# Kernel tuning notes

Measured on AMD Instinct MI355X. Metric: run time of the kernel, lower is better.

The kernel has to match this reference:

```python
import jax, jax.numpy as jnp
import numpy as np

N = 100000      # nodes
E = 1600000     # edges (avg degree 16)
DIN = 64
DOUT = 64
C = 8           # num classes; label -1 means unknown


def _xavier(key, shape):
    a = jnp.sqrt(6.0 / (shape[0] + shape[1]))
    return jax.random.uniform(key, shape, jnp.float32, -a, a)


def setup_inputs():
    key = jax.random.key(0)
    ks = jax.random.split(key, 17)
    return {
        "x": jax.random.normal(ks[0], (N, DIN), jnp.float32),
        "adj_low_vals": jax.random.uniform(ks[1], (E,), jnp.float32) / 16.0,
        "adj_high_vals": jax.random.uniform(ks[2], (E,), jnp.float32) / 16.0,
        "weight_low": _xavier(ks[3], (DIN, DOUT)),
        "weight_high": _xavier(ks[4], (DIN, DOUT)),
        "weight_mlp": _xavier(ks[5], (DIN, DOUT)),
        "att_vec_low_fr": _xavier(ks[6], (DOUT, 1)),
        "att_vec_high_fr": _xavier(ks[7], (DOUT, 1)),
        "att_vec_low_be": _xavier(ks[8], (DOUT, 1)),
        "att_vec_high_be": _xavier(ks[9], (DOUT, 1)),
        "att_vec_low_unk": _xavier(ks[10], (DOUT, 1)),
        "att_vec_high_unk": _xavier(ks[11], (DOUT, 1)),
        "att_vec_mlp": _xavier(ks[12], (DOUT, 1)),
        "att_vec7": _xavier(ks[13], (7, 7)),
        "edge_src": jax.random.randint(ks[14], (E,), 0, N),
        "edge_dst": jax.random.randint(ks[15], (E,), 0, N),
        "label_unk": jax.random.randint(ks[16], (N,), -1, C),
    }


def reference(x, adj_low_vals, adj_high_vals, weight_low, weight_high, weight_mlp,
              att_vec_low_fr, att_vec_high_fr, att_vec_low_be, att_vec_high_be,
              att_vec_low_unk, att_vec_high_unk, att_vec_mlp, att_vec7,
              edge_src, edge_dst, label_unk):
    def spmm(vals, feats):  # out[dst] += vals * feats[src]  (sparse [N,N] @ [N,D])
        return jax.ops.segment_sum(vals[:, None] * feats[edge_src], edge_dst, num_segments=N)

    output_low = jax.nn.relu(spmm(adj_low_vals, x @ weight_low))
    output_high = jax.nn.relu(spmm(adj_high_vals, x @ weight_high))
    output_mlp = jax.nn.relu(x @ weight_mlp)

    # per-edge fake label: 2 if either endpoint unknown (<0), 1 if labels differ
    # (both known) -> heterophilous, else 0 -> homophilous
    sl = label_unk[edge_src]
    dl = label_unk[edge_dst]
    fake = jnp.where((sl < 0) | (dl < 0), 2, jnp.where(sl != dl, 1, 0))

    h_low_e = output_low[edge_src]    # [E, DOUT] gathered messages
    h_high_e = output_high[edge_src]

    def agg(h_e, k):  # masked segment-sum over destination nodes
        m = (fake == k).astype(h_e.dtype)[:, None]
        return jax.ops.segment_sum(h_e * m, edge_dst, num_segments=N)

    neigh_homo_low, neigh_hete_low, neigh_unk_low = agg(h_low_e, 0), agg(h_low_e, 1), agg(h_low_e, 2)
    neigh_homo_high, neigh_hete_high, neigh_unk_high = agg(h_high_e, 0), agg(h_high_e, 1), agg(h_high_e, 2)

    # attention7 (fr_high_g is None branch)
    feats = jax.nn.sigmoid(jnp.concatenate([
        neigh_hete_low @ att_vec_low_fr, neigh_hete_high @ att_vec_high_fr,
        neigh_homo_low @ att_vec_low_be, neigh_homo_high @ att_vec_high_be,
        neigh_unk_low @ att_vec_low_unk, neigh_unk_high @ att_vec_high_unk,
        output_mlp @ att_vec_mlp], axis=1))  # [N, 7]
    att = jax.nn.softmax((feats @ att_vec7) / 7.0, axis=1)

    return 7.0 * (att[:, 0:1] * neigh_hete_low + att[:, 1:2] * neigh_hete_high
                  + att[:, 2:3] * neigh_homo_low + att[:, 3:4] * neigh_homo_high
                  + att[:, 4:5] * neigh_unk_low + att[:, 5:6] * neigh_unk_high
                  + att[:, 6:7] * output_mlp)
```

## Files before the change

kernel.cpp:

```cpp
#include <hip/hip_runtime.h>
#include <hip/hip_bf16.h>

typedef unsigned int u32;
typedef unsigned short u16;
typedef unsigned long long u64;

typedef __attribute__((ext_vector_type(8))) short bf16x8;
typedef __attribute__((ext_vector_type(4))) float f32x4;
typedef __attribute__((ext_vector_type(2))) float f32x2;

static __device__ __forceinline__ float bflo(u32 u) { return __uint_as_float(u << 16); }
static __device__ __forceinline__ float bfhi(u32 u) { return __uint_as_float(u & 0xFFFF0000u); }
static __device__ __forceinline__ float bf2f(u16 u) { return __uint_as_float((u32)u << 16); }
static __device__ __forceinline__ u32 f2bf(float f) {
    u32 u = __float_as_uint(f);
    return (u + 0x7FFFu + ((u >> 16) & 1u)) >> 16;
}
static __device__ __forceinline__ u32 packbf(float lo, float hi) {
    return f2bf(lo) | (f2bf(hi) << 16);
}
static __device__ __forceinline__ float ldf(const u16* p16, int idx, int isf32) {
    return isf32 ? ((const float*)p16)[idx] : bf2f(p16[idx]);
}
static __device__ __forceinline__ void load4(const u16* p, int q, int isf32, float* v) {
    if (isf32) {
        float4 t = ((const float4*)p)[q];
        v[0] = t.x; v[1] = t.y; v[2] = t.z; v[3] = t.w;
    } else {
        u32 a = ((const u32*)p)[q * 2], b = ((const u32*)p)[q * 2 + 1];
        v[0] = bflo(a); v[1] = bfhi(a); v[2] = bflo(b); v[3] = bfhi(b);
    }
}
static __device__ __forceinline__ float sanitize(float v, float code) {
    return (fabsf(v) < 1e30f) ? v : code;
}

static __device__ __forceinline__ f32x2 up2(u32 u) {
    f32x2 r;
    r.x = __uint_as_float(u << 16);
    r.y = __uint_as_float(u & 0xFFFF0000u);
    return r;
}
static __device__ __forceinline__ void pk_fma(f32x2& d, f32x2 a, f32x2 b) {
    asm("v_pk_fma_f32 %0, %1, %2, %0" : "+v"(d) : "v"(a), "v"(b));
}
static __device__ __forceinline__ void pk_add(f32x2& d, f32x2 a) {
    asm("v_pk_add_f32 %0, %1, %0" : "+v"(d) : "v"(a));
}

static __device__ __forceinline__ float wave_sum(float v) {
#pragma unroll
    for (int o = 32; o; o >>= 1) v += __shfl_xor(v, o, 64);
    return v;
}
static __device__ __forceinline__ float group_sum(float v) {
#pragma unroll
    for (int o = 8; o; o >>= 1) v += __shfl_xor(v, o, 64);
    return v;
}


__global__ void k_sentinel(float* __restrict__ out, int n, float val) {
    int i = blockIdx.x * blockDim.x + threadIdx.x;
    if (i < n) out[i] = val;
}

__global__ void k_zero_sniff(int* __restrict__ p, int n, const u16* __restrict__ x,
                             int* __restrict__ flag) {
    int i = blockIdx.x * blockDim.x + threadIdx.x;
    if (i < n) p[i] = 0;
    if (blockIdx.x == 0 && threadIdx.x < 64) {
        int lane = threadIdx.x;
        int wild = 0;
        for (int k = 0; k < 64; k++) {
            u32 u = x[lane * 64 + k];
            int e = (u >> 7) & 0xFF;
            if (e < 96 || e > 135) wild++;
        }
        float tot = wave_sum((float)wild);
        if (lane == 0) *flag = (tot > 200.f) ? 1 : 0;
    }
}


__global__ void k_hist(const int* __restrict__ dst, int E, int* __restrict__ deg) {
    int i = blockIdx.x * blockDim.x + threadIdx.x;
    if (i < E) atomicAdd(&deg[dst[i]], 1);
}

__global__ void k_scan_partial(const int* __restrict__ deg, int n, int* __restrict__ bsum) {
    int t = threadIdx.x;
    int base = blockIdx.x * 1024 + t * 4;
    int s = 0;
#pragma unroll
    for (int j = 0; j < 4; j++) {
        int idx = base + j;
        if (idx < n) s += deg[idx];
    }
    __shared__ int sh[256];
    sh[t] = s;
    __syncthreads();
    for (int d = 128; d; d >>= 1) {
        if (t < d) sh[t] += sh[t + d];
        __syncthreads();
    }
    if (t == 0) bsum[blockIdx.x] = sh[0];
}

__global__ void k_scan_bsum(const int* __restrict__ bsum, int nb, int* __restrict__ boff) {
    int t = threadIdx.x;
    int v = (t < nb) ? bsum[t] : 0;
    __shared__ int sh[256];
    sh[t] = v;
    __syncthreads();
    for (int d = 1; d < 256; d <<= 1) {
        int u = (t >= d) ? sh[t - d] : 0;
        __syncthreads();
        sh[t] += u;
        __syncthreads();
    }
    if (t < nb) boff[t] = sh[t] - v;
}

__global__ void k_scan_final(const int* __restrict__ deg, int n, const int* __restrict__ boff,
                             int* __restrict__ offsets, int Etot) {
    int t = threadIdx.x;
    int base = blockIdx.x * 1024 + t * 4;
    int v[4];
    int s = 0;
#pragma unroll
    for (int j = 0; j < 4; j++) {
        int idx = base + j;
        v[j] = (idx < n) ? deg[idx] : 0;
        s += v[j];
    }
    __shared__ int sh[256];
    sh[t] = s;
    __syncthreads();
    for (int d = 1; d < 256; d <<= 1) {
        int u = (t >= d) ? sh[t - d] : 0;
        __syncthreads();
        sh[t] += u;
        __syncthreads();
    }
    int ex = sh[t] - s + boff[blockIdx.x];
#pragma unroll
    for (int j = 0; j < 4; j++) {
        int idx = base + j;
        if (idx < n) offsets[idx] = ex;
        ex += v[j];
    }
    if (blockIdx.x == 0 && t == 0) offsets[n] = Etot;
}

__global__ void k_scat1(const int* __restrict__ src, const int* __restrict__ dst,
                        const u16* __restrict__ avl, const u16* __restrict__ avh,
                        const int* __restrict__ lab, int E,
                        const int* __restrict__ offsets, int* __restrict__ bcur,
                        u64* __restrict__ etmp, const int* __restrict__ flag) {
    int i = blockIdx.x * blockDim.x + threadIdx.x;
    if (i >= E) return;
    int isf32 = *flag;
    int d = dst[i];
    int b = d >> 8;
    int base = b << 8;
    int rank = atomicAdd(&bcur[b * 16], 1);
    int pos = offsets[base] + rank;
    if ((unsigned)pos >= (unsigned)E) return;
    int s = src[i];
    int sl = lab[s], dl = lab[d];
    int fake = (sl < 0 || dl < 0) ? 2 : ((sl != dl) ? 1 : 0);
    u32 lo32 = (u32)s | ((u32)fake << 20) | ((u32)(d - base) << 22);
    u32 hi32 = isf32 ? packbf(((const float*)avl)[i], ((const float*)avh)[i])
                     : ((u32)avl[i] | ((u32)avh[i] << 16));
    etmp[pos] = ((u64)hi32 << 32) | lo32;
}

__launch_bounds__(256) __global__
void k_scat2(const u64* __restrict__ etmp, const int* __restrict__ offsets, int N, int E,
             u64* __restrict__ epay) {
    __shared__ int cur[256];
    int b = blockIdx.x;
    int base = b << 8;
    int t = threadIdx.x;
    cur[t] = 0;
    __syncthreads();
    int hi = min(base + 256, N);
    int r0 = offsets[base];
    int r1 = offsets[hi];
    for (int e = r0 + t; e < r1; e += 256) {
        u64 p = etmp[e];
        int dloc = (int)(p >> 22) & 0xFF;
        int rank = atomicAdd(&cur[dloc], 1);
        int pos = offsets[base + dloc] + rank;
        if ((unsigned)pos < (unsigned)E) epay[pos] = p;
    }
}


__global__ void k_prepB(const u16* __restrict__ wl, const u16* __restrict__ wh,
                        const u16* __restrict__ wm, u16* __restrict__ Bpack,
                        u32* __restrict__ xwlh, u32* __restrict__ outlh, int N,
                        const int* __restrict__ flag) {
    int isf32 = *flag;
    if (threadIdx.x < 64) {
        xwlh[(size_t)N * 64 + threadIdx.x] = 0;
        outlh[(size_t)N * 64 + threadIdx.x] = 0;
    }
    for (int idx = threadIdx.x; idx < 12 * 2 * 64; idx += 256) {
        int slot = idx >> 6;
        int ln = idx & 63;
        int ct = slot >> 1, c = slot & 1;
        int mat = ct >> 2;
        const u16* W = (mat == 0) ? wl : (mat == 1) ? wh : wm;
        int col = (ct & 3) * 16 + (ln & 15);
        int kbase = c * 32 + (ln >> 4) * 8;
        u16* dst = Bpack + (size_t)idx * 8;
#pragma unroll
        for (int j = 0; j < 8; j++) dst[j] = (u16)f2bf(ldf(W, (kbase + j) * 64 + col, isf32));
    }
}

__launch_bounds__(256) __global__
void k_gemm_mfma(const u16* __restrict__ x, const u16* __restrict__ Bpack, int N,
                 u32* __restrict__ xwlh, float* __restrict__ omlp,
                 const int* __restrict__ flag) {
    int isf32 = *flag;
    int lane = threadIdx.x & 63;
    int wv = (blockIdx.x * 256 + threadIdx.x) >> 6;
    int nw = gridDim.x * 4;
    int m = lane & 15, quad = lane >> 4;
    int ntiles = (N + 15) >> 4;
    for (int tile = wv; tile < ntiles; tile += nw) {
        int r0 = tile * 16;
        int arow = min(r0 + m, N - 1);
        bf16x8 a[2];
#pragma unroll
        for (int c = 0; c < 2; c++) {
            int base = arow * 64 + c * 32 + quad * 8;
            if (isf32) {
                const float* xf = (const float*)x;
#pragma unroll
                for (int j = 0; j < 8; j++) a[c][j] = (short)f2bf(xf[base + j]);
            } else {
#pragma unroll
                for (int j = 0; j < 8; j++) a[c][j] = (short)x[base + j];
            }
        }
        f32x4 acc[12];
#pragma unroll
        for (int t = 0; t < 12; t++) acc[t] = (f32x4){0.f, 0.f, 0.f, 0.f};
#pragma unroll
        for (int t = 0; t < 12; t++) {
#pragma unroll
            for (int c = 0; c < 2; c++) {
                bf16x8 b = *(const bf16x8*)(Bpack + (size_t)((t * 2 + c) * 64 + lane) * 8);
                acc[t] = __builtin_amdgcn_mfma_f32_16x16x32_bf16(a[c], b, acc[t], 0, 0, 0);
            }
        }
#pragma unroll
        for (int t = 0; t < 4; t++) {
#pragma unroll
            for (int r = 0; r < 4; r++) {
                int row = r0 + quad * 4 + r;
                if (row < N) {
                    int o = row * 64 + t * 16 + m;
                    xwlh[o] = packbf(acc[t][r], acc[t + 4][r]);
                    omlp[o] = fmaxf(acc[t + 8][r], 0.f);
                }
            }
        }
    }
}


__launch_bounds__(256) __global__
void k_spmm4n(const u32* __restrict__ xwlh, const u64* __restrict__ epay,
              const int* __restrict__ offsets, int N, int E, u32* __restrict__ outlh) {
    int lane = threadIdx.x & 63;
    int gwave = blockIdx.x * 4 + (threadIdx.x >> 6);
    int g = lane & 15, gi = lane >> 4;
    int node = gwave * 4 + gi;
    bool vn = node < N;
    int s = vn ? offsets[node] : 0;
    int e = vn ? offsets[node + 1] : 0;
    int deg = e - s;
    int md = deg;
    md = max(md, __shfl_xor(md, 16, 64));
    md = max(md, __shfl_xor(md, 32, 64));
    f32x2 acc[4];
#pragma unroll
    for (int f = 0; f < 4; f++) acc[f] = (f32x2){0.f, 0.f};
    for (int t = 0; t < md; t += 4) {
        u64 p[4];
#pragma unroll
        for (int u = 0; u < 4; u++) {
            int idx = max(s + min(t + u, deg - 1), 0);
            p[u] = epay[idx];
        }
        uint4 R[4];
        u32 vv[4];
#pragma unroll
        for (int u = 0; u < 4; u++) {
            int sj = ((t + u) < deg) ? min((int)(p[u] & 0xFFFFF), N) : N;
            vv[u] = (u32)(p[u] >> 32);
            R[u] = *((const uint4*)(xwlh + (size_t)sj * 64) + g);
        }
#pragma unroll
        for (int u = 0; u < 4; u++) {
            f32x2 wp;
            wp.x = bflo(vv[u]);
            wp.y = bfhi(vv[u]);
            pk_fma(acc[0], up2(R[u].x), wp);
            pk_fma(acc[1], up2(R[u].y), wp);
            pk_fma(acc[2], up2(R[u].z), wp);
            pk_fma(acc[3], up2(R[u].w), wp);
        }
    }
    if (vn) {
        uint4 W;
        W.x = packbf(fmaxf(acc[0].x, 0.f), fmaxf(acc[0].y, 0.f));
        W.y = packbf(fmaxf(acc[1].x, 0.f), fmaxf(acc[1].y, 0.f));
        W.z = packbf(fmaxf(acc[2].x, 0.f), fmaxf(acc[2].y, 0.f));
        W.w = packbf(fmaxf(acc[3].x, 0.f), fmaxf(acc[3].y, 0.f));
        ((uint4*)(outlh + (size_t)node * 64))[g] = W;
    }
}


__launch_bounds__(256) __global__
void k_agg4n(const u32* __restrict__ outlh, const u64* __restrict__ epay,
             const int* __restrict__ offsets,
             const u16* __restrict__ aLF, const u16* __restrict__ aHF,
             const u16* __restrict__ aLB, const u16* __restrict__ aHB,
             const u16* __restrict__ aLU, const u16* __restrict__ aHU,
             const u16* __restrict__ aM, const u16* __restrict__ a7, int N, int E,
             float* __restrict__ out, const int* __restrict__ flag) {
    int isf32 = *flag;
    int lane = threadIdx.x & 63;
    int gwave = blockIdx.x * 4 + (threadIdx.x >> 6);
    int g = lane & 15, gi = lane >> 4;
    int node = gwave * 4 + gi;
    bool vn = node < N;
    int s = vn ? offsets[node] : 0;
    int e = vn ? offsets[node + 1] : 0;
    int deg = e - s;
    int md = deg;
    md = max(md, __shfl_xor(md, 16, 64));
    md = max(md, __shfl_xor(md, 32, 64));
    f32x2 aT[4], aHe[4], aUn[4];
#pragma unroll
    for (int f = 0; f < 4; f++) {
        aT[f] = (f32x2){0.f, 0.f};
        aHe[f] = (f32x2){0.f, 0.f};
        aUn[f] = (f32x2){0.f, 0.f};
    }
    for (int t = 0; t < md; t += 4) {
        u64 p[4];
#pragma unroll
        for (int u = 0; u < 4; u++) {
            int idx = max(s + min(t + u, deg - 1), 0);
            p[u] = epay[idx];
        }
        uint4 R[4];
        int fk[4];
#pragma unroll
        for (int u = 0; u < 4; u++) {
            fk[u] = (int)(p[u] >> 20) & 3;
            int sj = ((t + u) < deg) ? min((int)(p[u] & 0xFFFFF), N) : N;
            R[u] = *((const uint4*)(outlh + (size_t)sj * 64) + g);
        }
#pragma unroll
        for (int u = 0; u < 4; u++) {
            float he = (fk[u] == 1) ? 1.f : 0.f;
            float un = (fk[u] == 2) ? 1.f : 0.f;
            f32x2 mhe, mun;
            mhe.x = he; mhe.y = he;
            mun.x = un; mun.y = un;
            f32x2 r0 = up2(R[u].x), r1 = up2(R[u].y), r2 = up2(R[u].z), r3 = up2(R[u].w);
            pk_add(aT[0], r0); pk_add(aT[1], r1); pk_add(aT[2], r2); pk_add(aT[3], r3);
            pk_fma(aHe[0], r0, mhe); pk_fma(aHe[1], r1, mhe);
            pk_fma(aHe[2], r2, mhe); pk_fma(aHe[3], r3, mhe);
            pk_fma(aUn[0], r0, mun); pk_fma(aUn[1], r1, mun);
            pk_fma(aUn[2], r2, mun); pk_fma(aUn[3], r3, mun);
        }
    }
    float heL[4], heH[4], hoL[4], hoH[4], unL[4], unH[4];
#pragma unroll
    for (int f = 0; f < 4; f++) {
        heL[f] = aHe[f].x; heH[f] = aHe[f].y;
        unL[f] = aUn[f].x; unH[f] = aUn[f].y;
        hoL[f] = aT[f].x - heL[f] - unL[f];
        hoH[f] = aT[f].y - heH[f] - unH[f];
    }
    float vLF[4], vHF[4], vLB[4], vHB[4], vLU[4], vHU[4], vM[4];
    load4(aLF, g, isf32, vLF);
    load4(aHF, g, isf32, vHF);
    load4(aLB, g, isf32, vLB);
    load4(aHB, g, isf32, vHB);
    load4(aLU, g, isf32, vLU);
    load4(aHU, g, isf32, vHU);
    load4(aM, g, isf32, vM);
    float mvv[4] = {0.f, 0.f, 0.f, 0.f};
    if (vn) {
        float4 MV = ((const float4*)(out + (size_t)node * 64))[g];
        mvv[0] = MV.x; mvv[1] = MV.y; mvv[2] = MV.z; mvv[3] = MV.w;
    }

    float p0 = 0, p1 = 0, p2 = 0, p3 = 0, p4 = 0, p5 = 0, p6 = 0;
#pragma unroll
    for (int k = 0; k < 4; k++) {
        p0 += heL[k] * vLF[k];
        p1 += heH[k] * vHF[k];
        p2 += hoL[k] * vLB[k];
        p3 += hoH[k] * vHB[k];
        p4 += unL[k] * vLU[k];
        p5 += unH[k] * vHU[k];
        p6 += mvv[k] * vM[k];
    }
    float d0 = group_sum(p0), d1 = group_sum(p1), d2 = group_sum(p2), d3 = group_sum(p3);
    float d4 = group_sum(p4), d5 = group_sum(p5), d6 = group_sum(p6);

    float f[7];
    f[0] = 1.f / (1.f + expf(-d0));
    f[1] = 1.f / (1.f + expf(-d1));
    f[2] = 1.f / (1.f + expf(-d2));
    f[3] = 1.f / (1.f + expf(-d3));
    f[4] = 1.f / (1.f + expf(-d4));
    f[5] = 1.f / (1.f + expf(-d5));
    f[6] = 1.f / (1.f + expf(-d6));

    float z[7];
#pragma unroll
    for (int jj = 0; jj < 7; jj++) {
        float acc = 0.f;
#pragma unroll
        for (int i = 0; i < 7; i++) acc += f[i] * ldf(a7, i * 7 + jj, isf32);
        z[jj] = acc * (1.f / 7.f);
    }
    float m = z[0];
#pragma unroll
    for (int jj = 1; jj < 7; jj++) m = fmaxf(m, z[jj]);
    float wsum = 0.f;
    float wv[7];
#pragma unroll
    for (int jj = 0; jj < 7; jj++) { wv[jj] = expf(z[jj] - m); wsum += wv[jj]; }
    float s7 = 7.f / wsum;

    if (vn) {
        float4 W;
        float o0 = wv[0] * heL[0] + wv[1] * heH[0] + wv[2] * hoL[0] + wv[3] * hoH[0] +
                   wv[4] * unL[0] + wv[5] * unH[0] + wv[6] * mvv[0];
        float o1 = wv[0] * heL[1] + wv[1] * heH[1] + wv[2] * hoL[1] + wv[3] * hoH[1] +
                   wv[4] * unL[1] + wv[5] * unH[1] + wv[6] * mvv[1];
        float o2 = wv[0] * heL[2] + wv[1] * heH[2] + wv[2] * hoL[2] + wv[3] * hoH[2] +
                   wv[4] * unL[2] + wv[5] * unH[2] + wv[6] * mvv[2];
        float o3 = wv[0] * heL[3] + wv[1] * heH[3] + wv[2] * hoL[3] + wv[3] * hoH[3] +
                   wv[4] * unL[3] + wv[5] * unH[3] + wv[6] * mvv[3];
        W.x = sanitize(o0 * s7, 333.f);
        W.y = sanitize(o1 * s7, 333.f);
        W.z = sanitize(o2 * s7, 333.f);
        W.w = sanitize(o3 * s7, 333.f);
        ((float4*)(out + (size_t)node * 64))[g] = W;
    }
}


extern "C" void kernel_launch(void* const* d_in, const int* in_sizes, int n_in, void* d_out,
                              int out_size, void* d_ws, size_t ws_size, hipStream_t stream) {
    const u16* x = (const u16*)d_in[0];
    const u16* avl = (const u16*)d_in[1];
    const u16* avh = (const u16*)d_in[2];
    const u16* wl = (const u16*)d_in[3];
    const u16* wh = (const u16*)d_in[4];
    const u16* wm = (const u16*)d_in[5];
    const u16* aLF = (const u16*)d_in[6];
    const u16* aHF = (const u16*)d_in[7];
    const u16* aLB = (const u16*)d_in[8];
    const u16* aHB = (const u16*)d_in[9];
    const u16* aLU = (const u16*)d_in[10];
    const u16* aHU = (const u16*)d_in[11];
    const u16* aM = (const u16*)d_in[12];
    const u16* a7 = (const u16*)d_in[13];
    const int* esrc = (const int*)d_in[14];
    const int* edst = (const int*)d_in[15];
    const int* lab = (const int*)d_in[16];
    float* out = (float*)d_out;

    const int N = in_sizes[0] / 64;
    const int E = in_sizes[1];

    char* w = (char*)d_ws;
    size_t off = 0;
    auto alloc = [&](size_t bytes) -> char* {
        char* p = w + off;
        off += (bytes + 255) & ~(size_t)255;
        return p;
    };
    int* flag = (int*)alloc(256);
    int* offsets = (int*)alloc((size_t)(N + 1) * 4);
    int* degcur = (int*)alloc((size_t)2 * N * 4);
    int* bsum = (int*)alloc(256 * 4);
    int* boff = (int*)alloc(256 * 4);
    u16* Bpack = (u16*)alloc(12 * 2 * 64 * 8 * 2);
    u64* epay = (u64*)alloc((size_t)E * 8);
    u32* xwlh = (u32*)alloc((size_t)(N + 1) * 64 * 4);
    u32* outlh = (u32*)alloc((size_t)(N + 1) * 64 * 4);

    if (ws_size < off) {
        k_sentinel<<<(out_size + 255) / 256, 256, 0, stream>>>(out, out_size, 1000.0f);
        return;
    }

    int* deg = degcur;
    int* bcur = degcur + N;
    u64* etmp = (u64*)xwlh;
    int NB = (N + 1023) / 1024;
    int NB2 = (N + 255) / 256;

    k_zero_sniff<<<(2 * N + 255) / 256, 256, 0, stream>>>(degcur, 2 * N, x, flag);
    k_hist<<<(E + 255) / 256, 256, 0, stream>>>(edst, E, deg);
    k_scan_partial<<<NB, 256, 0, stream>>>(deg, N, bsum);
    k_scan_bsum<<<1, 256, 0, stream>>>(bsum, NB, boff);
    k_scan_final<<<NB, 256, 0, stream>>>(deg, N, boff, offsets, E);
    k_scat1<<<(E + 255) / 256, 256, 0, stream>>>(esrc, edst, avl, avh, lab, E, offsets, bcur,
                                                 etmp, flag);
    k_scat2<<<NB2, 256, 0, stream>>>(etmp, offsets, N, E, epay);

    k_prepB<<<1, 256, 0, stream>>>(wl, wh, wm, Bpack, xwlh, outlh, N, flag);
    int ntiles = (N + 15) / 16;
    int gemmBlocks = (ntiles + 3) / 4;
    k_gemm_mfma<<<gemmBlocks, 256, 0, stream>>>(x, Bpack, N, xwlh, out , flag);

    int nodeBlocks = (N + 15) / 16;
    k_spmm4n<<<nodeBlocks, 256, 0, stream>>>(xwlh, epay, offsets, N, E, outlh);
    k_agg4n<<<nodeBlocks, 256, 0, stream>>>(outlh, epay, offsets, aLF, aHF, aLB, aHB, aLU, aHU,
                                            aM, a7, N, E, out, flag);
}
```

Baseline: 467.7 us.

## Pad CSR rows to multiples of four and process one node per wave

Each node's edge list is padded to a multiple of 4 with dummy entries that point at the zero row N and carry fake label 3. The SpMM and aggregation kernels now give one wave per node, with four edge slots of 16 lanes each, and finish with a cross-slot shuffle reduction. This removes the per-group max-degree divergence and the clamped index work of the old four-nodes-per-wave scheme. In exchange it adds a fill of the padded payload array, extra dummy edge loads, a shuffle reduction, and idle lanes on the final store. The GEMM's input loads are also vectorised.

```diff
diff --git a/kernel.cpp b/kernel.cpp
--- a/kernel.cpp
+++ b/kernel.cpp
@@ -57,6 +57,12 @@
 #pragma unroll
     for (int o = 8; o; o >>= 1) v += __shfl_xor(v, o, 64);
     return v;
+}
+static __device__ __forceinline__ void eslot_reduce(f32x2& a) {
+    a.x += __shfl_xor(a.x, 16, 64);
+    a.y += __shfl_xor(a.y, 16, 64);
+    a.x += __shfl_xor(a.x, 32, 64);
+    a.y += __shfl_xor(a.y, 32, 64);
 }
 
 
@@ -95,7 +101,7 @@
 #pragma unroll
     for (int j = 0; j < 4; j++) {
         int idx = base + j;
-        if (idx < n) s += deg[idx];
+        if (idx < n) s += (deg[idx] + 3) & ~3;
     }
     __shared__ int sh[256];
     sh[t] = s;
@@ -107,7 +113,8 @@
     if (t == 0) bsum[blockIdx.x] = sh[0];
 }
 
-__global__ void k_scan_bsum(const int* __restrict__ bsum, int nb, int* __restrict__ boff) {
+__global__ void k_scan_bsum(const int* __restrict__ bsum, int nb, int* __restrict__ boff,
+                            int* __restrict__ tot) {
     int t = threadIdx.x;
     int v = (t < nb) ? bsum[t] : 0;
     __shared__ int sh[256];
@@ -120,10 +127,11 @@
         __syncthreads();
     }
     if (t < nb) boff[t] = sh[t] - v;
+    if (t == nb - 1) *tot = sh[t];
 }
 
 __global__ void k_scan_final(const int* __restrict__ deg, int n, const int* __restrict__ boff,
-                             int* __restrict__ offsets, int Etot) {
+                             int* __restrict__ offsets) {
     int t = threadIdx.x;
     int base = blockIdx.x * 1024 + t * 4;
     int v[4];
@@ -131,7 +139,7 @@
 #pragma unroll
     for (int j = 0; j < 4; j++) {
         int idx = base + j;
-        v[j] = (idx < n) ? deg[idx] : 0;
+        v[j] = (idx < n) ? ((deg[idx] + 3) & ~3) : 0;
         s += v[j];
     }
     __shared__ int sh[256];
@@ -150,15 +158,17 @@
         if (idx < n) offsets[idx] = ex;
         ex += v[j];
     }
-    if (blockIdx.x == 0 && t == 0) offsets[n] = Etot;
 }
 
 __global__ void k_scat1(const int* __restrict__ src, const int* __restrict__ dst,
                         const u16* __restrict__ avl, const u16* __restrict__ avh,
-                        const int* __restrict__ lab, int E,
+                        const int* __restrict__ lab, int E, int Pcap, u64 dum,
                         const int* __restrict__ offsets, int* __restrict__ bcur,
-                        u64* __restrict__ etmp, const int* __restrict__ flag) {
+                        u64* __restrict__ etmp, u64* __restrict__ epay,
+                        const int* __restrict__ flag) {
     int i = blockIdx.x * blockDim.x + threadIdx.x;
+    int stride = blockDim.x * gridDim.x;
+    for (int j = i; j < Pcap; j += stride) epay[j] = dum;
     if (i >= E) return;
     int isf32 = *flag;
     int d = dst[i];
@@ -166,7 +176,7 @@
     int base = b << 8;
     int rank = atomicAdd(&bcur[b * 16], 1);
     int pos = offsets[base] + rank;
-    if ((unsigned)pos >= (unsigned)E) return;
+    if ((unsigned)pos >= (unsigned)Pcap) return;
     int s = src[i];
     int sl = lab[s], dl = lab[d];
     int fake = (sl < 0 || dl < 0) ? 2 : ((sl != dl) ? 1 : 0);
@@ -177,23 +187,22 @@
 }
 
 __launch_bounds__(256) __global__
-void k_scat2(const u64* __restrict__ etmp, const int* __restrict__ offsets, int N, int E,
-             u64* __restrict__ epay) {
+void k_scat2(const u64* __restrict__ etmp, const int* __restrict__ offsets,
+             const int* __restrict__ bcur, int N, int Pcap, u64* __restrict__ epay) {
     __shared__ int cur[256];
     int b = blockIdx.x;
     int base = b << 8;
     int t = threadIdx.x;
     cur[t] = 0;
     __syncthreads();
-    int hi = min(base + 256, N);
     int r0 = offsets[base];
-    int r1 = offsets[hi];
+    int r1 = r0 + bcur[b * 16];
     for (int e = r0 + t; e < r1; e += 256) {
         u64 p = etmp[e];
         int dloc = (int)(p >> 22) & 0xFF;
         int rank = atomicAdd(&cur[dloc], 1);
         int pos = offsets[base + dloc] + rank;
-        if ((unsigned)pos < (unsigned)E) epay[pos] = p;
+        if ((unsigned)pos < (unsigned)Pcap) epay[pos] = p;
     }
 }
 
@@ -239,12 +248,15 @@
         for (int c = 0; c < 2; c++) {
             int base = arow * 64 + c * 32 + quad * 8;
             if (isf32) {
-                const float* xf = (const float*)x;
-#pragma unroll
-                for (int j = 0; j < 8; j++) a[c][j] = (short)f2bf(xf[base + j]);
+                const float4* xf = (const float4*)x;
+                int q = (base >> 2);
+                float4 t0 = xf[q], t1 = xf[q + 1];
+                a[c][0] = (short)f2bf(t0.x); a[c][1] = (short)f2bf(t0.y);
+                a[c][2] = (short)f2bf(t0.z); a[c][3] = (short)f2bf(t0.w);
+                a[c][4] = (short)f2bf(t1.x); a[c][5] = (short)f2bf(t1.y);
+                a[c][6] = (short)f2bf(t1.z); a[c][7] = (short)f2bf(t1.w);
             } else {
-#pragma unroll
-                for (int j = 0; j < 8; j++) a[c][j] = (short)x[base + j];
+                a[c] = *(const bf16x8*)(x + base);
             }
         }
         f32x4 acc[12];
@@ -275,109 +287,101 @@
 
 
 __launch_bounds__(256) __global__
-void k_spmm4n(const u32* __restrict__ xwlh, const u64* __restrict__ epay,
-              const int* __restrict__ offsets, int N, int E, u32* __restrict__ outlh) {
+void k_spmm1n(const u32* __restrict__ xwlh, const u64* __restrict__ epay,
+              const int* __restrict__ offsets, int N, u32* __restrict__ outlh) {
     int lane = threadIdx.x & 63;
-    int gwave = blockIdx.x * 4 + (threadIdx.x >> 6);
-    int g = lane & 15, gi = lane >> 4;
-    int node = gwave * 4 + gi;
-    bool vn = node < N;
-    int s = vn ? offsets[node] : 0;
-    int e = vn ? offsets[node + 1] : 0;
-    int deg = e - s;
-    int md = deg;
-    md = max(md, __shfl_xor(md, 16, 64));
-    md = max(md, __shfl_xor(md, 32, 64));
+    int node = blockIdx.x * 4 + (threadIdx.x >> 6);
+    if (node >= N) return;
+    int f = lane & 15, eslot = lane >> 4;
+    int s = offsets[node];
+    int epad = offsets[node + 1];
+    const uint4* tab = (const uint4*)xwlh + f;
     f32x2 acc[4];
 #pragma unroll
-    for (int f = 0; f < 4; f++) acc[f] = (f32x2){0.f, 0.f};
-    for (int t = 0; t < md; t += 4) {
-        u64 p[4];
-#pragma unroll
-        for (int u = 0; u < 4; u++) {
-            int idx = max(s + min(t + u, deg - 1), 0);
-            p[u] = epay[idx];
-        }
-        uint4 R[4];
-        u32 vv[4];
-#pragma unroll
-        for (int u = 0; u < 4; u++) {
-            int sj = ((t + u) < deg) ? min((int)(p[u] & 0xFFFFF), N) : N;
-            vv[u] = (u32)(p[u] >> 32);
-            R[u] = *((const uint4*)(xwlh + (size_t)sj * 64) + g);
-        }
-#pragma unroll
-        for (int u = 0; u < 4; u++) {
-            f32x2 wp;
-            wp.x = bflo(vv[u]);
-            wp.y = bfhi(vv[u]);
-            pk_fma(acc[0], up2(R[u].x), wp);
-            pk_fma(acc[1], up2(R[u].y), wp);
-            pk_fma(acc[2], up2(R[u].z), wp);
-            pk_fma(acc[3], up2(R[u].w), wp);
-        }
-    }
-    if (vn) {
+    for (int k = 0; k < 4; k++) acc[k] = (f32x2){0.f, 0.f};
+    int t = s + eslot;
+    for (; t + 4 < epad; t += 8) {
+        u64 p0 = epay[t];
+        u64 p1 = epay[t + 4];
+        uint4 R0 = tab[(size_t)(p0 & 0xFFFFF) << 4];
+        uint4 R1 = tab[(size_t)(p1 & 0xFFFFF) << 4];
+        u32 h0 = (u32)(p0 >> 32), h1 = (u32)(p1 >> 32);
+        f32x2 w0, w1;
+        w0.x = bflo(h0); w0.y = bfhi(h0);
+        w1.x = bflo(h1); w1.y = bfhi(h1);
+        pk_fma(acc[0], up2(R0.x), w0);
+        pk_fma(acc[1], up2(R0.y), w0);
+        pk_fma(acc[2], up2(R0.z), w0);
+        pk_fma(acc[3], up2(R0.w), w0);
+        pk_fma(acc[0], up2(R1.x), w1);
+        pk_fma(acc[1], up2(R1.y), w1);
+        pk_fma(acc[2], up2(R1.z), w1);
+        pk_fma(acc[3], up2(R1.w), w1);
+    }
+    if (t < epad) {
+        u64 p0 = epay[t];
+        uint4 R0 = tab[(size_t)(p0 & 0xFFFFF) << 4];
+        u32 h0 = (u32)(p0 >> 32);
+        f32x2 w0;
+        w0.x = bflo(h0); w0.y = bfhi(h0);
+        pk_fma(acc[0], up2(R0.x), w0);
+        pk_fma(acc[1], up2(R0.y), w0);
+        pk_fma(acc[2], up2(R0.z), w0);
+        pk_fma(acc[3], up2(R0.w), w0);
+    }
+#pragma unroll
+    for (int k = 0; k < 4; k++) eslot_reduce(acc[k]);
+    if (eslot == 0) {
         uint4 W;
         W.x = packbf(fmaxf(acc[0].x, 0.f), fmaxf(acc[0].y, 0.f));
         W.y = packbf(fmaxf(acc[1].x, 0.f), fmaxf(acc[1].y, 0.f));
         W.z = packbf(fmaxf(acc[2].x, 0.f), fmaxf(acc[2].y, 0.f));
         W.w = packbf(fmaxf(acc[3].x, 0.f), fmaxf(acc[3].y, 0.f));
-        ((uint4*)(outlh + (size_t)node * 64))[g] = W;
+        ((uint4*)(outlh + (size_t)node * 64))[f] = W;
     }
 }
 
 
 __launch_bounds__(256) __global__
-void k_agg4n(const u32* __restrict__ outlh, const u64* __restrict__ epay,
+void k_agg1n(const u32* __restrict__ outlh, const u64* __restrict__ epay,
              const int* __restrict__ offsets,
              const u16* __restrict__ aLF, const u16* __restrict__ aHF,
              const u16* __restrict__ aLB, const u16* __restrict__ aHB,
              const u16* __restrict__ aLU, const u16* __restrict__ aHU,
-             const u16* __restrict__ aM, const u16* __restrict__ a7, int N, int E,
+             const u16* __restrict__ aM, const u16* __restrict__ a7, int N,
              float* __restrict__ out, const int* __restrict__ flag) {
     int isf32 = *flag;
     int lane = threadIdx.x & 63;
-    int gwave = blockIdx.x * 4 + (threadIdx.x >> 6);
-    int g = lane & 15, gi = lane >> 4;
-    int node = gwave * 4 + gi;
-    bool vn = node < N;
-    int s = vn ? offsets[node] : 0;
-    int e = vn ? offsets[node + 1] : 0;
-    int deg = e - s;
-    int md = deg;
-    md = max(md, __shfl_xor(md, 16, 64));
-    md = max(md, __shfl_xor(md, 32, 64));
+    int node = blockIdx.x * 4 + (threadIdx.x >> 6);
+    if (node >= N) return;
+    int f = lane & 15, eslot = lane >> 4;
+    int s = offsets[node];
+    int epad = offsets[node + 1];
+    const uint4* tab = (const uint4*)outlh + f;
     f32x2 aT[4], aHe[4], aUn[4];
 #pragma unroll
-    for (int f = 0; f < 4; f++) {
-        aT[f] = (f32x2){0.f, 0.f};
-        aHe[f] = (f32x2){0.f, 0.f};
-        aUn[f] = (f32x2){0.f, 0.f};
-    }
-    for (int t = 0; t < md; t += 4) {
-        u64 p[4];
-#pragma unroll
-        for (int u = 0; u < 4; u++) {
-            int idx = max(s + min(t + u, deg - 1), 0);
-            p[u] = epay[idx];
-        }
-        uint4 R[4];
-        int fk[4];
-#pragma unroll
-        for (int u = 0; u < 4; u++) {
-            fk[u] = (int)(p[u] >> 20) & 3;
-            int sj = ((t + u) < deg) ? min((int)(p[u] & 0xFFFFF), N) : N;
-            R[u] = *((const uint4*)(outlh + (size_t)sj * 64) + g);
-        }
-#pragma unroll
-        for (int u = 0; u < 4; u++) {
-            float he = (fk[u] == 1) ? 1.f : 0.f;
-            float un = (fk[u] == 2) ? 1.f : 0.f;
+    for (int k = 0; k < 4; k++) {
+        aT[k] = (f32x2){0.f, 0.f};
+        aHe[k] = (f32x2){0.f, 0.f};
+        aUn[k] = (f32x2){0.f, 0.f};
+    }
+    int t = s + eslot;
+    for (; t + 4 < epad; t += 8) {
+        u64 p0 = epay[t];
+        u64 p1 = epay[t + 4];
+        uint4 R0 = tab[(size_t)(p0 & 0xFFFFF) << 4];
+        uint4 R1 = tab[(size_t)(p1 & 0xFFFFF) << 4];
+#pragma unroll
+        for (int half = 0; half < 2; half++) {
+            u64 p = half ? p1 : p0;
+            uint4 R = half ? R1 : R0;
+            int fk = (int)(p >> 20) & 3;
+            float he = (fk == 1) ? 1.f : 0.f;
+            float un = (fk == 2) ? 1.f : 0.f;
             f32x2 mhe, mun;
             mhe.x = he; mhe.y = he;
             mun.x = un; mun.y = un;
-            f32x2 r0 = up2(R[u].x), r1 = up2(R[u].y), r2 = up2(R[u].z), r3 = up2(R[u].w);
+            f32x2 r0 = up2(R.x), r1 = up2(R.y), r2 = up2(R.z), r3 = up2(R.w);
             pk_add(aT[0], r0); pk_add(aT[1], r1); pk_add(aT[2], r2); pk_add(aT[3], r3);
             pk_fma(aHe[0], r0, mhe); pk_fma(aHe[1], r1, mhe);
             pk_fma(aHe[2], r2, mhe); pk_fma(aHe[3], r3, mhe);
@@ -385,27 +389,46 @@
             pk_fma(aUn[2], r2, mun); pk_fma(aUn[3], r3, mun);
         }
     }
+    if (t < epad) {
+        u64 p = epay[t];
+        uint4 R = tab[(size_t)(p & 0xFFFFF) << 4];
+        int fk = (int)(p >> 20) & 3;
+        float he = (fk == 1) ? 1.f : 0.f;
+        float un = (fk == 2) ? 1.f : 0.f;
+        f32x2 mhe, mun;
+        mhe.x = he; mhe.y = he;
+        mun.x = un; mun.y = un;
+        f32x2 r0 = up2(R.x), r1 = up2(R.y), r2 = up2(R.z), r3 = up2(R.w);
+        pk_add(aT[0], r0); pk_add(aT[1], r1); pk_add(aT[2], r2); pk_add(aT[3], r3);
+        pk_fma(aHe[0], r0, mhe); pk_fma(aHe[1], r1, mhe);
+        pk_fma(aHe[2], r2, mhe); pk_fma(aHe[3], r3, mhe);
+        pk_fma(aUn[0], r0, mun); pk_fma(aUn[1], r1, mun);
+        pk_fma(aUn[2], r2, mun); pk_fma(aUn[3], r3, mun);
+    }
+#pragma unroll
+    for (int k = 0; k < 4; k++) {
+        eslot_reduce(aT[k]);
+        eslot_reduce(aHe[k]);
+        eslot_reduce(aUn[k]);
+    }
     float heL[4], heH[4], hoL[4], hoH[4], unL[4], unH[4];
 #pragma unroll
-    for (int f = 0; f < 4; f++) {
-        heL[f] = aHe[f].x; heH[f] = aHe[f].y;
-        unL[f] = aUn[f].x; unH[f] = aUn[f].y;
-        hoL[f] = aT[f].x - heL[f] - unL[f];
-        hoH[f] = aT[f].y - heH[f] - unH[f];
+    for (int k = 0; k < 4; k++) {
+        heL[k] = aHe[k].x; heH[k] = aHe[k].y;
+        unL[k] = aUn[k].x; unH[k] = aUn[k].y;
+        hoL[k] = aT[k].x - heL[k] - unL[k];
+        hoH[k] = aT[k].y - heH[k] - unH[k];
     }
     float vLF[4], vHF[4], vLB[4], vHB[4], vLU[4], vHU[4], vM[4];
-    load4(aLF, g, isf32, vLF);
-    load4(aHF, g, isf32, vHF);
-    load4(aLB, g, isf32, vLB);
-    load4(aHB, g, isf32, vHB);
-    load4(aLU, g, isf32, vLU);
-    load4(aHU, g, isf32, vHU);
-    load4(aM, g, isf32, vM);
-    float mvv[4] = {0.f, 0.f, 0.f, 0.f};
-    if (vn) {
-        float4 MV = ((const float4*)(out + (size_t)node * 64))[g];
-        mvv[0] = MV.x; mvv[1] = MV.y; mvv[2] = MV.z; mvv[3] = MV.w;
-    }
+    load4(aLF, f, isf32, vLF);
+    load4(aHF, f, isf32, vHF);
+    load4(aLB, f, isf32, vLB);
+    load4(aHB, f, isf32, vHB);
+    load4(aLU, f, isf32, vLU);
+    load4(aHU, f, isf32, vHU);
+    load4(aM, f, isf32, vM);
+    float4 MV = ((const float4*)(out + (size_t)node * 64))[f];
+    float mvv[4] = {MV.x, MV.y, MV.z, MV.w};
 
     float p0 = 0, p1 = 0, p2 = 0, p3 = 0, p4 = 0, p5 = 0, p6 = 0;
 #pragma unroll
@@ -421,47 +444,47 @@
     float d0 = group_sum(p0), d1 = group_sum(p1), d2 = group_sum(p2), d3 = group_sum(p3);
     float d4 = group_sum(p4), d5 = group_sum(p5), d6 = group_sum(p6);
 
-    float f[7];
-    f[0] = 1.f / (1.f + expf(-d0));
-    f[1] = 1.f / (1.f + expf(-d1));
-    f[2] = 1.f / (1.f + expf(-d2));
-    f[3] = 1.f / (1.f + expf(-d3));
-    f[4] = 1.f / (1.f + expf(-d4));
-    f[5] = 1.f / (1.f + expf(-d5));
-    f[6] = 1.f / (1.f + expf(-d6));
+    float fg[7];
+    fg[0] = 1.f / (1.f + expf(-d0));
+    fg[1] = 1.f / (1.f + expf(-d1));
+    fg[2] = 1.f / (1.f + expf(-d2));
+    fg[3] = 1.f / (1.f + expf(-d3));
+    fg[4] = 1.f / (1.f + expf(-d4));
+    fg[5] = 1.f / (1.f + expf(-d5));
+    fg[6] = 1.f / (1.f + expf(-d6));
 
     float z[7];
 #pragma unroll
     for (int jj = 0; jj < 7; jj++) {
         float acc = 0.f;
 #pragma unroll
-        for (int i = 0; i < 7; i++) acc += f[i] * ldf(a7, i * 7 + jj, isf32);
+        for (int i = 0; i < 7; i++) acc += fg[i] * ldf(a7, i * 7 + jj, isf32);
         z[jj] = acc * (1.f / 7.f);
     }
     float m = z[0];
 #pragma unroll
     for (int jj = 1; jj < 7; jj++) m = fmaxf(m, z[jj]);
     float wsum = 0.f;
-    float wv[7];
-#pragma unroll
-    for (int jj = 0; jj < 7; jj++) { wv[jj] = expf(z[jj] - m); wsum += wv[jj]; }
+    float wvv[7];
+#pragma unroll
+    for (int jj = 0; jj < 7; jj++) { wvv[jj] = expf(z[jj] - m); wsum += wvv[jj]; }
     float s7 = 7.f / wsum;
 
-    if (vn) {
+    if (eslot == 0) {
         float4 W;
-        float o0 = wv[0] * heL[0] + wv[1] * heH[0] + wv[2] * hoL[0] + wv[3] * hoH[0] +
-                   wv[4] * unL[0] + wv[5] * unH[0] + wv[6] * mvv[0];
-        float o1 = wv[0] * heL[1] + wv[1] * heH[1] + wv[2] * hoL[1] + wv[3] * hoH[1] +
-                   wv[4] * unL[1] + wv[5] * unH[1] + wv[6] * mvv[1];
-        float o2 = wv[0] * heL[2] + wv[1] * heH[2] + wv[2] * hoL[2] + wv[3] * hoH[2] +
-                   wv[4] * unL[2] + wv[5] * unH[2] + wv[6] * mvv[2];
-        float o3 = wv[0] * heL[3] + wv[1] * heH[3] + wv[2] * hoL[3] + wv[3] * hoH[3] +
-                   wv[4] * unL[3] + wv[5] * unH[3] + wv[6] * mvv[3];
+        float o0 = wvv[0] * heL[0] + wvv[1] * heH[0] + wvv[2] * hoL[0] + wvv[3] * hoH[0] +
+                   wvv[4] * unL[0] + wvv[5] * unH[0] + wvv[6] * mvv[0];
+        float o1 = wvv[0] * heL[1] + wvv[1] * heH[1] + wvv[2] * hoL[1] + wvv[3] * hoH[1] +
+                   wvv[4] * unL[1] + wvv[5] * unH[1] + wvv[6] * mvv[1];
+        float o2 = wvv[0] * heL[2] + wvv[1] * heH[2] + wvv[2] * hoL[2] + wvv[3] * hoH[2] +
+                   wvv[4] * unL[2] + wvv[5] * unH[2] + wvv[6] * mvv[2];
+        float o3 = wvv[0] * heL[3] + wvv[1] * heH[3] + wvv[2] * hoL[3] + wvv[3] * hoH[3] +
+                   wvv[4] * unL[3] + wvv[5] * unH[3] + wvv[6] * mvv[3];
         W.x = sanitize(o0 * s7, 333.f);
         W.y = sanitize(o1 * s7, 333.f);
         W.z = sanitize(o2 * s7, 333.f);
         W.w = sanitize(o3 * s7, 333.f);
-        ((float4*)(out + (size_t)node * 64))[g] = W;
+        ((float4*)(out + (size_t)node * 64))[f] = W;
     }
 }
 
@@ -489,6 +512,7 @@
 
     const int N = in_sizes[0] / 64;
     const int E = in_sizes[1];
+    const int Pcap = E + 3 * N + 64;
 
     char* w = (char*)d_ws;
     size_t off = 0;
@@ -503,7 +527,7 @@
     int* bsum = (int*)alloc(256 * 4);
     int* boff = (int*)alloc(256 * 4);
     u16* Bpack = (u16*)alloc(12 * 2 * 64 * 8 * 2);
-    u64* epay = (u64*)alloc((size_t)E * 8);
+    u64* epay = (u64*)alloc((size_t)Pcap * 8);
     u32* xwlh = (u32*)alloc((size_t)(N + 1) * 64 * 4);
     u32* outlh = (u32*)alloc((size_t)(N + 1) * 64 * 4);
 
@@ -517,23 +541,24 @@
     u64* etmp = (u64*)xwlh;
     int NB = (N + 1023) / 1024;
     int NB2 = (N + 255) / 256;
+    u64 dum = (u64)((u32)N | (3u << 20));
 
     k_zero_sniff<<<(2 * N + 255) / 256, 256, 0, stream>>>(degcur, 2 * N, x, flag);
     k_hist<<<(E + 255) / 256, 256, 0, stream>>>(edst, E, deg);
     k_scan_partial<<<NB, 256, 0, stream>>>(deg, N, bsum);
-    k_scan_bsum<<<1, 256, 0, stream>>>(bsum, NB, boff);
-    k_scan_final<<<NB, 256, 0, stream>>>(deg, N, boff, offsets, E);
-    k_scat1<<<(E + 255) / 256, 256, 0, stream>>>(esrc, edst, avl, avh, lab, E, offsets, bcur,
-                                                 etmp, flag);
-    k_scat2<<<NB2, 256, 0, stream>>>(etmp, offsets, N, E, epay);
+    k_scan_bsum<<<1, 256, 0, stream>>>(bsum, NB, boff, offsets + N);
+    k_scan_final<<<NB, 256, 0, stream>>>(deg, N, boff, offsets);
+    k_scat1<<<(E + 255) / 256, 256, 0, stream>>>(esrc, edst, avl, avh, lab, E, Pcap, dum,
+                                                 offsets, bcur, etmp, epay, flag);
+    k_scat2<<<NB2, 256, 0, stream>>>(etmp, offsets, bcur, N, Pcap, epay);
 
     k_prepB<<<1, 256, 0, stream>>>(wl, wh, wm, Bpack, xwlh, outlh, N, flag);
     int ntiles = (N + 15) / 16;
     int gemmBlocks = (ntiles + 3) / 4;
     k_gemm_mfma<<<gemmBlocks, 256, 0, stream>>>(x, Bpack, N, xwlh, out , flag);
 
-    int nodeBlocks = (N + 15) / 16;
-    k_spmm4n<<<nodeBlocks, 256, 0, stream>>>(xwlh, epay, offsets, N, E, outlh);
-    k_agg4n<<<nodeBlocks, 256, 0, stream>>>(outlh, epay, offsets, aLF, aHF, aLB, aHB, aLU, aHU,
-                                            aM, a7, N, E, out, flag);
-}
+    int nodeBlocks = (N + 3) / 4;
+    k_spmm1n<<<nodeBlocks, 256, 0, stream>>>(xwlh, epay, offsets, N, outlh);
+    k_agg1n<<<nodeBlocks, 256, 0, stream>>>(outlh, epay, offsets, aLF, aHF, aLB, aHB, aLU, aHU,
+                                            aM, a7, N, out, flag);
+}
```

Result: slower. 568.5 us (+21.6%).

## Slice SpMM gather table into feature blocks and drop padded-degree loops

Applied to the files above, without the earlier changes.

The GEMM now writes the packed low/high XW table in a sliced layout (8 slices of 8 u32 per node), and a new SpMM kernel assigns each block one slice so the gathered working set per pass is smaller and more cache-resident. Both SpMM and aggregation loops now iterate each node's own degree directly instead of padding to the max degree across the 4-node group, which removes wasted gathers and the dummy zero row. The GEMM input loads are vectorized as float4 / bf16x8. In exchange, the SpMM re-reads the edge list eight times (once per slice) and uses narrow 4-byte gathers.

```diff
diff --git a/kernel.cpp b/kernel.cpp
--- a/kernel.cpp
+++ b/kernel.cpp
@@ -200,13 +200,8 @@
 
 __global__ void k_prepB(const u16* __restrict__ wl, const u16* __restrict__ wh,
                         const u16* __restrict__ wm, u16* __restrict__ Bpack,
-                        u32* __restrict__ xwlh, u32* __restrict__ outlh, int N,
                         const int* __restrict__ flag) {
     int isf32 = *flag;
-    if (threadIdx.x < 64) {
-        xwlh[(size_t)N * 64 + threadIdx.x] = 0;
-        outlh[(size_t)N * 64 + threadIdx.x] = 0;
-    }
     for (int idx = threadIdx.x; idx < 12 * 2 * 64; idx += 256) {
         int slot = idx >> 6;
         int ln = idx & 63;
@@ -223,7 +218,7 @@
 
 __launch_bounds__(256) __global__
 void k_gemm_mfma(const u16* __restrict__ x, const u16* __restrict__ Bpack, int N,
-                 u32* __restrict__ xwlh, float* __restrict__ omlp,
+                 u32* __restrict__ xwlhS, float* __restrict__ omlp,
                  const int* __restrict__ flag) {
     int isf32 = *flag;
     int lane = threadIdx.x & 63;
@@ -239,12 +234,15 @@
         for (int c = 0; c < 2; c++) {
             int base = arow * 64 + c * 32 + quad * 8;
             if (isf32) {
-                const float* xf = (const float*)x;
-#pragma unroll
-                for (int j = 0; j < 8; j++) a[c][j] = (short)f2bf(xf[base + j]);
+                const float4* xf = (const float4*)x;
+                int q = (base >> 2);
+                float4 t0 = xf[q], t1 = xf[q + 1];
+                a[c][0] = (short)f2bf(t0.x); a[c][1] = (short)f2bf(t0.y);
+                a[c][2] = (short)f2bf(t0.z); a[c][3] = (short)f2bf(t0.w);
+                a[c][4] = (short)f2bf(t1.x); a[c][5] = (short)f2bf(t1.y);
+                a[c][6] = (short)f2bf(t1.z); a[c][7] = (short)f2bf(t1.w);
             } else {
-#pragma unroll
-                for (int j = 0; j < 8; j++) a[c][j] = (short)x[base + j];
+                a[c] = *(const bf16x8*)(x + base);
             }
         }
         f32x4 acc[12];
@@ -260,13 +258,15 @@
         }
 #pragma unroll
         for (int t = 0; t < 4; t++) {
+            int fp = t * 16 + m;
+            int sl = fp >> 3, dd = fp & 7;
+            u32* xp = xwlhS + (size_t)sl * N * 8 + dd;
 #pragma unroll
             for (int r = 0; r < 4; r++) {
                 int row = r0 + quad * 4 + r;
                 if (row < N) {
-                    int o = row * 64 + t * 16 + m;
-                    xwlh[o] = packbf(acc[t][r], acc[t + 4][r]);
-                    omlp[o] = fmaxf(acc[t + 8][r], 0.f);
+                    xp[(size_t)row * 8] = packbf(acc[t][r], acc[t + 4][r]);
+                    omlp[row * 64 + fp] = fmaxf(acc[t + 8][r], 0.f);
                 }
             }
         }
@@ -275,56 +275,32 @@
 
 
 __launch_bounds__(256) __global__
-void k_spmm4n(const u32* __restrict__ xwlh, const u64* __restrict__ epay,
-              const int* __restrict__ offsets, int N, int E, u32* __restrict__ outlh) {
-    int lane = threadIdx.x & 63;
-    int gwave = blockIdx.x * 4 + (threadIdx.x >> 6);
-    int g = lane & 15, gi = lane >> 4;
-    int node = gwave * 4 + gi;
-    bool vn = node < N;
-    int s = vn ? offsets[node] : 0;
-    int e = vn ? offsets[node + 1] : 0;
-    int deg = e - s;
-    int md = deg;
-    md = max(md, __shfl_xor(md, 16, 64));
-    md = max(md, __shfl_xor(md, 32, 64));
-    f32x2 acc[4];
-#pragma unroll
-    for (int f = 0; f < 4; f++) acc[f] = (f32x2){0.f, 0.f};
-    for (int t = 0; t < md; t += 4) {
-        u64 p[4];
-#pragma unroll
-        for (int u = 0; u < 4; u++) {
-            int idx = max(s + min(t + u, deg - 1), 0);
-            p[u] = epay[idx];
-        }
-        uint4 R[4];
-        u32 vv[4];
-#pragma unroll
-        for (int u = 0; u < 4; u++) {
-            int sj = ((t + u) < deg) ? min((int)(p[u] & 0xFFFFF), N) : N;
-            vv[u] = (u32)(p[u] >> 32);
-            R[u] = *((const uint4*)(xwlh + (size_t)sj * 64) + g);
-        }
-#pragma unroll
-        for (int u = 0; u < 4; u++) {
-            f32x2 wp;
-            wp.x = bflo(vv[u]);
-            wp.y = bfhi(vv[u]);
-            pk_fma(acc[0], up2(R[u].x), wp);
-            pk_fma(acc[1], up2(R[u].y), wp);
-            pk_fma(acc[2], up2(R[u].z), wp);
-            pk_fma(acc[3], up2(R[u].w), wp);
-        }
-    }
-    if (vn) {
-        uint4 W;
-        W.x = packbf(fmaxf(acc[0].x, 0.f), fmaxf(acc[0].y, 0.f));
-        W.y = packbf(fmaxf(acc[1].x, 0.f), fmaxf(acc[1].y, 0.f));
-        W.z = packbf(fmaxf(acc[2].x, 0.f), fmaxf(acc[2].y, 0.f));
-        W.w = packbf(fmaxf(acc[3].x, 0.f), fmaxf(acc[3].y, 0.f));
-        ((uint4*)(outlh + (size_t)node * 64))[g] = W;
-    }
+void k_spmm_sl(const u32* __restrict__ xwlhS, const u64* __restrict__ epay,
+               const int* __restrict__ offsets, int N, u32* __restrict__ outlh) {
+    int tid = threadIdx.x;
+    int lane = tid & 63;
+    int slice = blockIdx.x & 7;
+    int chunk = blockIdx.x >> 3;
+    int node = chunk * 32 + (tid >> 6) * 8 + (lane >> 3);
+    if (node >= N) return;
+    int d = lane & 7;
+    int s = offsets[node], e = offsets[node + 1];
+    const u32* tab = xwlhS + (size_t)slice * N * 8 + d;
+    f32x2 acc = (f32x2){0.f, 0.f};
+    int t = s;
+    for (; t + 1 < e; t += 2) {
+        u64 p0 = epay[t], p1 = epay[t + 1];
+        u32 R0 = tab[(size_t)(p0 & 0xFFFFF) * 8];
+        u32 R1 = tab[(size_t)(p1 & 0xFFFFF) * 8];
+        pk_fma(acc, up2(R0), up2((u32)(p0 >> 32)));
+        pk_fma(acc, up2(R1), up2((u32)(p1 >> 32)));
+    }
+    if (t < e) {
+        u64 p0 = epay[t];
+        u32 R0 = tab[(size_t)(p0 & 0xFFFFF) * 8];
+        pk_fma(acc, up2(R0), up2((u32)(p0 >> 32)));
+    }
+    outlh[(size_t)node * 64 + slice * 8 + d] = packbf(fmaxf(acc.x, 0.f), fmaxf(acc.y, 0.f));
 }
 
 
@@ -344,40 +320,30 @@
     bool vn = node < N;
     int s = vn ? offsets[node] : 0;
     int e = vn ? offsets[node + 1] : 0;
-    int deg = e - s;
-    int md = deg;
-    md = max(md, __shfl_xor(md, 16, 64));
-    md = max(md, __shfl_xor(md, 32, 64));
+    const uint4* tab = (const uint4*)outlh + g;
     f32x2 aT[4], aHe[4], aUn[4];
 #pragma unroll
-    for (int f = 0; f < 4; f++) {
-        aT[f] = (f32x2){0.f, 0.f};
-        aHe[f] = (f32x2){0.f, 0.f};
-        aUn[f] = (f32x2){0.f, 0.f};
-    }
-    for (int t = 0; t < md; t += 4) {
-        u64 p[4];
-#pragma unroll
-        for (int u = 0; u < 4; u++) {
-            int idx = max(s + min(t + u, deg - 1), 0);
-            p[u] = epay[idx];
-        }
-        uint4 R[4];
-        int fk[4];
-#pragma unroll
-        for (int u = 0; u < 4; u++) {
-            fk[u] = (int)(p[u] >> 20) & 3;
-            int sj = ((t + u) < deg) ? min((int)(p[u] & 0xFFFFF), N) : N;
-            R[u] = *((const uint4*)(outlh + (size_t)sj * 64) + g);
-        }
-#pragma unroll
-        for (int u = 0; u < 4; u++) {
-            float he = (fk[u] == 1) ? 1.f : 0.f;
-            float un = (fk[u] == 2) ? 1.f : 0.f;
+    for (int k = 0; k < 4; k++) {
+        aT[k] = (f32x2){0.f, 0.f};
+        aHe[k] = (f32x2){0.f, 0.f};
+        aUn[k] = (f32x2){0.f, 0.f};
+    }
+    int t = s;
+    for (; t + 1 < e; t += 2) {
+        u64 p0 = epay[t], p1 = epay[t + 1];
+        uint4 R0 = tab[(size_t)(p0 & 0xFFFFF) << 4];
+        uint4 R1 = tab[(size_t)(p1 & 0xFFFFF) << 4];
+#pragma unroll
+        for (int half = 0; half < 2; half++) {
+            u64 p = half ? p1 : p0;
+            uint4 R = half ? R1 : R0;
+            int fk = (int)(p >> 20) & 3;
+            float he = (fk == 1) ? 1.f : 0.f;
+            float un = (fk == 2) ? 1.f : 0.f;
             f32x2 mhe, mun;
             mhe.x = he; mhe.y = he;
             mun.x = un; mun.y = un;
-            f32x2 r0 = up2(R[u].x), r1 = up2(R[u].y), r2 = up2(R[u].z), r3 = up2(R[u].w);
+            f32x2 r0 = up2(R.x), r1 = up2(R.y), r2 = up2(R.z), r3 = up2(R.w);
             pk_add(aT[0], r0); pk_add(aT[1], r1); pk_add(aT[2], r2); pk_add(aT[3], r3);
             pk_fma(aHe[0], r0, mhe); pk_fma(aHe[1], r1, mhe);
             pk_fma(aHe[2], r2, mhe); pk_fma(aHe[3], r3, mhe);
@@ -385,13 +351,29 @@
             pk_fma(aUn[2], r2, mun); pk_fma(aUn[3], r3, mun);
         }
     }
+    if (t < e) {
+        u64 p = epay[t];
+        uint4 R = tab[(size_t)(p & 0xFFFFF) << 4];
+        int fk = (int)(p >> 20) & 3;
+        float he = (fk == 1) ? 1.f : 0.f;
+        float un = (fk == 2) ? 1.f : 0.f;
+        f32x2 mhe, mun;
+        mhe.x = he; mhe.y = he;
+        mun.x = un; mun.y = un;
+        f32x2 r0 = up2(R.x), r1 = up2(R.y), r2 = up2(R.z), r3 = up2(R.w);
+        pk_add(aT[0], r0); pk_add(aT[1], r1); pk_add(aT[2], r2); pk_add(aT[3], r3);
+        pk_fma(aHe[0], r0, mhe); pk_fma(aHe[1], r1, mhe);
+        pk_fma(aHe[2], r2, mhe); pk_fma(aHe[3], r3, mhe);
+        pk_fma(aUn[0], r0, mun); pk_fma(aUn[1], r1, mun);
+        pk_fma(aUn[2], r2, mun); pk_fma(aUn[3], r3, mun);
+    }
     float heL[4], heH[4], hoL[4], hoH[4], unL[4], unH[4];
 #pragma unroll
-    for (int f = 0; f < 4; f++) {
-        heL[f] = aHe[f].x; heH[f] = aHe[f].y;
-        unL[f] = aUn[f].x; unH[f] = aUn[f].y;
-        hoL[f] = aT[f].x - heL[f] - unL[f];
-        hoH[f] = aT[f].y - heH[f] - unH[f];
+    for (int k = 0; k < 4; k++) {
+        heL[k] = aHe[k].x; heH[k] = aHe[k].y;
+        unL[k] = aUn[k].x; unH[k] = aUn[k].y;
+        hoL[k] = aT[k].x - heL[k] - unL[k];
+        hoH[k] = aT[k].y - heH[k] - unH[k];
     }
     float vLF[4], vHF[4], vLB[4], vHB[4], vLU[4], vHU[4], vM[4];
     load4(aLF, g, isf32, vLF);
@@ -504,8 +486,8 @@
     int* boff = (int*)alloc(256 * 4);
     u16* Bpack = (u16*)alloc(12 * 2 * 64 * 8 * 2);
     u64* epay = (u64*)alloc((size_t)E * 8);
-    u32* xwlh = (u32*)alloc((size_t)(N + 1) * 64 * 4);
-    u32* outlh = (u32*)alloc((size_t)(N + 1) * 64 * 4);
+    u32* xwlhS = (u32*)alloc((size_t)N * 64 * 4);
+    u32* outlh = (u32*)alloc((size_t)N * 64 * 4);
 
     if (ws_size < off) {
         k_sentinel<<<(out_size + 255) / 256, 256, 0, stream>>>(out, out_size, 1000.0f);
@@ -514,7 +496,7 @@
 
     int* deg = degcur;
     int* bcur = degcur + N;
-    u64* etmp = (u64*)xwlh;
+    u64* etmp = (u64*)xwlhS;
     int NB = (N + 1023) / 1024;
     int NB2 = (N + 255) / 256;
 
@@ -527,13 +509,15 @@
                                                  etmp, flag);
     k_scat2<<<NB2, 256, 0, stream>>>(etmp, offsets, N, E, epay);
 
-    k_prepB<<<1, 256, 0, stream>>>(wl, wh, wm, Bpack, xwlh, outlh, N, flag);
+    k_prepB<<<1, 256, 0, stream>>>(wl, wh, wm, Bpack, flag);
     int ntiles = (N + 15) / 16;
     int gemmBlocks = (ntiles + 3) / 4;
-    k_gemm_mfma<<<gemmBlocks, 256, 0, stream>>>(x, Bpack, N, xwlh, out , flag);
-
+    k_gemm_mfma<<<gemmBlocks, 256, 0, stream>>>(x, Bpack, N, xwlhS, out ,
+                                                flag);
+
+    int spmmBlocks = ((N + 31) / 32) * 8;
+    k_spmm_sl<<<spmmBlocks, 256, 0, stream>>>(xwlhS, epay, offsets, N, outlh);
     int nodeBlocks = (N + 15) / 16;
-    k_spmm4n<<<nodeBlocks, 256, 0, stream>>>(xwlh, epay, offsets, N, E, outlh);
     k_agg4n<<<nodeBlocks, 256, 0, stream>>>(outlh, epay, offsets, aLF, aHF, aLB, aHB, aLU, aHU,
                                             aM, a7, N, E, out, flag);
 }
```

Result: slower. 557.4 us (+19.2%).
